# Optimization experiments

Hardware: AMD Instinct MI355X
Metric: run time of the kernel (lower is better)

Reference implementation:

```python
import jax, jax.numpy as jnp
import numpy as np

# CTBG circuit dims: units=[512,512,512], action_sz=6
UNIT1, UNIT2, UNIT3, ACTION = 512, 512, 512, 6
D_GPE_IN = UNIT1 * 3          # 1536  (striatum D1/D2/D3 blocks)
D_GPE_OUT = UNIT2 * 3         # 1536
D_GPI_IN = (UNIT1 + UNIT2) * 3  # 3072 (striatum + GPe/STN blocks)
D_GPI_OUT = UNIT2 * 3         # 1536
B = 16384


def setup_inputs() -> dict:
    key = jax.random.key(0)
    ks = jax.random.split(key, 12)
    x = jax.random.normal(ks[0], (B, D_GPE_IN), jnp.float32)
    # per-unit diagonal connectivity masks (unit_diags): [units, input_dim]
    gpe_mask = jax.random.bernoulli(ks[1], 0.5, (D_GPE_OUT, D_GPE_IN)).astype(jnp.float32)
    gpi_mask = jax.random.bernoulli(ks[2], 0.5, (D_GPI_OUT, D_GPI_IN)).astype(jnp.float32)
    # non-negative weights, uniform [0, 0.01) as in the TF initializer
    gpe_w = jax.random.uniform(ks[3], (D_GPE_IN, D_GPE_OUT), jnp.float32, 0.0, 0.01)
    gpe_b = jnp.zeros((D_GPE_OUT,), jnp.float32)
    gpi_w = jax.random.uniform(ks[4], (D_GPI_IN, D_GPI_OUT), jnp.float32, 0.0, 0.01)
    gpi_b = jnp.zeros((D_GPI_OUT,), jnp.float32)
    # Motor_cortex dense stack
    w1 = jax.random.normal(ks[5], (D_GPI_OUT, UNIT3), jnp.float32) / np.sqrt(D_GPI_OUT)
    b1 = jnp.zeros((UNIT3,), jnp.float32)
    w2 = jax.random.normal(ks[6], (UNIT3, UNIT3), jnp.float32) / np.sqrt(UNIT3)
    b2 = jnp.zeros((UNIT3,), jnp.float32)
    w3 = jax.random.normal(ks[7], (UNIT3, ACTION), jnp.float32) / np.sqrt(UNIT3)
    b3 = jnp.zeros((ACTION,), jnp.float32)
    return {"x": x, "gpe_mask": gpe_mask, "gpe_w": gpe_w, "gpe_b": gpe_b,
            "gpi_mask": gpi_mask, "gpi_w": gpi_w, "gpi_b": gpi_b,
            "w1": w1, "b1": b1, "w2": w2, "b2": b2, "w3": w3, "b3": b3}


def _masked_layer(x, mask, w, b):
    # TF original: p = transpose(matmul(diag(mask_u), x^T)) -> [B,U,I];
    #              f = diag_part(matmul(p, w)) + b
    # algebraically: f[b,u] = sum_i mask[u,i] * x[b,i] * w[i,u] + b[u]
    # which is a plain matmul against the element-wise masked weight.
    return x @ (w * mask.T) + b


def reference(x, gpe_mask, gpe_w, gpe_b, gpi_mask, gpi_w, gpi_b,
              w1, b1, w2, b2, w3, b3):
    gpe_out = _masked_layer(x, gpe_mask, gpe_w, gpe_b)          # [B, 1536]
    gpi_in = jnp.concatenate([x, gpe_out], axis=-1)              # [B, 3072]
    gpi_out = _masked_layer(gpi_in, gpi_mask, gpi_w, gpi_b)      # [B, 1536]
    h = jax.nn.relu(gpi_out @ w1 + b1)
    h = jax.nn.relu(h @ w2 + b2)
    return jax.nn.relu(h @ w3 + b3)                              # [B, 6]
```

## Files before the change

kernel.cpp:

```cpp
#include <hip/hip_runtime.h>
#include <stdint.h>


typedef __attribute__((ext_vector_type(8))) short short8;
typedef __attribute__((ext_vector_type(4))) float floatx4;

typedef const __attribute__((address_space(1))) void* gas1_cvp;
typedef __attribute__((address_space(3))) void* gas3_vp;

__device__ __forceinline__ void load_lds16(const void* g, void* s) {
    __builtin_amdgcn_global_load_lds((gas1_cvp)g, (gas3_vp)s, 16, 0, 0);
}

__device__ __forceinline__ unsigned short f2bf(float f) {
    unsigned int u = __float_as_uint(f);
    u = u + 0x7fffu + ((u >> 16) & 1u);
    return (unsigned short)(u >> 16);
}
__device__ __forceinline__ float bf2f(unsigned short h) {
    return __uint_as_float(((unsigned int)h) << 16);
}

__global__ void convert_x_kernel(const float* __restrict__ x,
                                 unsigned short* __restrict__ xb) {
    int idx = blockIdx.x * blockDim.x + threadIdx.x;
    int e = idx * 4;
    float4 v = *(const float4*)(x + e);
    ushort4 o;
    o.x = f2bf(v.x); o.y = f2bf(v.y); o.z = f2bf(v.z); o.w = f2bf(v.w);
    *(ushort4*)(xb + e) = o;
}

__device__ __forceinline__ void dev_prep_t(
        float (*tile)[65],
        const float* __restrict__ w, const float* __restrict__ mask,
        unsigned short* __restrict__ out,
        int ldw, int ldm, int ldo, int bx, int by) {
    int n0 = bx * 64;
    int k0 = by * 64;
    int t = threadIdx.x;
    int c4 = (t & 15) * 4;
    int r  = t >> 4;

    #pragma unroll
    for (int p = 0; p < 4; ++p) {
        int kk = r + p * 16;
        float4 v = *(const float4*)(w + (size_t)(k0 + kk) * ldw + n0 + c4);
        tile[c4 + 0][kk] = v.x;
        tile[c4 + 1][kk] = v.y;
        tile[c4 + 2][kk] = v.z;
        tile[c4 + 3][kk] = v.w;
    }
    __syncthreads();
    #pragma unroll
    for (int p = 0; p < 4; ++p) {
        int nn = r + p * 16;
        float mx = 1.f, my = 1.f, mz = 1.f, mw = 1.f;
        if (mask) {
            float4 m = *(const float4*)(mask + (size_t)(n0 + nn) * ldm + k0 + c4);
            mx = m.x; my = m.y; mz = m.z; mw = m.w;
        }
        ushort4 o;
        o.x = f2bf(tile[nn][c4 + 0] * mx);
        o.y = f2bf(tile[nn][c4 + 1] * my);
        o.z = f2bf(tile[nn][c4 + 2] * mz);
        o.w = f2bf(tile[nn][c4 + 3] * mw);
        *(ushort4*)(out + (size_t)(n0 + nn) * ldo + k0 + c4) = o;
    }
}

__device__ __forceinline__ void dev_prep_nt(
        float (*tile)[65],
        const float* __restrict__ w, const float* __restrict__ mask,
        unsigned short* __restrict__ out,
        int ldw, int ldm, int ldo, int bx, int by) {
    int j0 = bx * 64;
    int i0 = by * 64;
    int t = threadIdx.x;
    int c4 = (t & 15) * 4;
    int r  = t >> 4;

    #pragma unroll
    for (int p = 0; p < 4; ++p) {
        int jj = r + p * 16;
        float4 m = *(const float4*)(mask + (size_t)(j0 + jj) * ldm + i0 + c4);
        tile[c4 + 0][jj] = m.x;
        tile[c4 + 1][jj] = m.y;
        tile[c4 + 2][jj] = m.z;
        tile[c4 + 3][jj] = m.w;
    }
    __syncthreads();
    #pragma unroll
    for (int p = 0; p < 4; ++p) {
        int ii = r + p * 16;
        float4 v = *(const float4*)(w + (size_t)(i0 + ii) * ldw + j0 + c4);
        ushort4 o;
        o.x = f2bf(v.x * tile[ii][c4 + 0]);
        o.y = f2bf(v.y * tile[ii][c4 + 1]);
        o.z = f2bf(v.z * tile[ii][c4 + 2]);
        o.w = f2bf(v.w * tile[ii][c4 + 3]);
        *(ushort4*)(out + (size_t)(i0 + ii) * ldo + j0 + c4) = o;
    }
}

__global__ __launch_bounds__(256) void prep_all_kernel(
        const float* __restrict__ gpe_w, const float* __restrict__ gpe_mask,
        const float* __restrict__ gpi_w, const float* __restrict__ gpi_mask,
        const float* __restrict__ w1, const float* __restrict__ w2,
        unsigned short* __restrict__ wi_topnt, unsigned short* __restrict__ wi_bot,
        unsigned short* __restrict__ we_nt, unsigned short* __restrict__ w1t,
        unsigned short* __restrict__ w2t) {
    __shared__ float tile[64][65];
    int b = blockIdx.x;
    if (b < 576) {
        dev_prep_nt(tile, gpi_w, gpi_mask, wi_topnt, 1536, 3072, 1536,
                    b % 24, b / 24);
    } else if (b < 1152) {
        int lb = b - 576;
        dev_prep_t(tile, gpi_w + (size_t)1536 * 1536, gpi_mask + 1536, wi_bot,
                   1536, 3072, 1536, lb % 24, lb / 24);
    } else if (b < 1728) {
        int lb = b - 1152;
        dev_prep_nt(tile, gpe_w, gpe_mask, we_nt, 1536, 1536, 1536,
                    lb % 24, lb / 24);
    } else if (b < 1920) {
        int lb = b - 1728;
        dev_prep_t(tile, w1, nullptr, w1t, 512, 0, 1536, lb % 8, lb / 8);
    } else {
        int lb = b - 1920;
        dev_prep_t(tile, w2, nullptr, w2t, 512, 0, 512, lb % 8, lb / 8);
    }
}

__global__ void bvec_kernel(const float* __restrict__ avec,
                            const float* __restrict__ base,
                            const unsigned short* __restrict__ wbt,
                            float* __restrict__ outv, int K, int ld) {
    int u = blockIdx.x * 4 + (threadIdx.x >> 6);
    int lane = threadIdx.x & 63;
    const unsigned short* rowp = wbt + (size_t)u * ld;
    float s = 0.f;
    for (int j = lane; j < K; j += 64) s += avec[j] * bf2f(rowp[j]);
    #pragma unroll
    for (int off = 32; off; off >>= 1) s += __shfl_down(s, off, 64);
    if (lane == 0) outv[u] = base[u] + s;
}

template <int BMODE>
__global__ __launch_bounds__(256) void gemm64_kernel(
        const unsigned short* __restrict__ A,
        const unsigned short* __restrict__ Bt,
        const float* __restrict__ bias,
        const unsigned short* __restrict__ Add,
        unsigned short* __restrict__ C,
        int K, int lda, int ldc) {
    __shared__ unsigned short As[64 * 32];
    __shared__ unsigned short Bs[64 * 32];

    const int m0 = blockIdx.y * 64;
    const int n0 = blockIdx.x * 64;
    const int t    = threadIdx.x;
    const int lane = t & 63;
    const int w    = t >> 6;
    const int wm   = w >> 1;
    const int wn   = w & 1;
    const int lm   = lane & 15;
    const int lq   = lane >> 4;

    const int srow = lane >> 2;
    const int scol = (lane & 3) * 8;
    const unsigned short* ag = A  + (size_t)(m0 + w * 16 + srow) * lda + scol;
    const unsigned short* bg = Bt + (size_t)(n0 + w * 16 + srow) * K + scol;
    unsigned short* sA = As + w * 512;
    unsigned short* sB = Bs + w * 512;

    const unsigned short* arp[2];
    const unsigned short* brp[2];
    #pragma unroll
    for (int i = 0; i < 2; ++i) {
        arp[i] = As + (wm * 32 + i * 16 + lm) * 32 + lq * 8;
        brp[i] = Bs + (wn * 32 + i * 16 + lm) * 32 + lq * 8;
    }

    floatx4 acc[2][2] = {};

    for (int k0 = 0; k0 < K; k0 += 32) {
        __syncthreads();
        load_lds16(ag + k0, sA);
        load_lds16(bg + k0, sB);
        __syncthreads();

        short8 af[2], bf8[2];
        #pragma unroll
        for (int i = 0; i < 2; ++i) {
            af[i]  = *(const short8*)arp[i];
            bf8[i] = *(const short8*)brp[i];
        }
        #pragma unroll
        for (int mi = 0; mi < 2; ++mi)
            #pragma unroll
            for (int ni = 0; ni < 2; ++ni)
                acc[mi][ni] = __builtin_amdgcn_mfma_f32_16x16x32_bf16(
                    af[mi], bf8[ni], acc[mi][ni], 0, 0, 0);
    }

    float bv[2] = {0.f, 0.f};
    if (BMODE == 0) {
        #pragma unroll
        for (int ni = 0; ni < 2; ++ni) bv[ni] = bias[n0 + wn * 32 + ni * 16 + lm];
    }

    #pragma unroll
    for (int mi = 0; mi < 2; ++mi) {
        int rbase = m0 + wm * 32 + mi * 16 + lq * 4;
        #pragma unroll
        for (int ni = 0; ni < 2; ++ni) {
            int cc = n0 + wn * 32 + ni * 16 + lm;
            #pragma unroll
            for (int r = 0; r < 4; ++r) {
                float v = acc[mi][ni][r];
                if (BMODE == 1) v += bf2f(Add[(size_t)(rbase + r) * ldc + cc]);
                if (BMODE == 0) v += bv[ni];
                C[(size_t)(rbase + r) * ldc + cc] = f2bf(v);
            }
        }
    }
}

template <bool RELU>
__global__ __launch_bounds__(256) void gemm_bt_kernel(
        const unsigned short* __restrict__ A,
        const unsigned short* __restrict__ Bt,
        const float* __restrict__ bias,
        unsigned short* __restrict__ C,
        int K, int lda, int ldc) {
    __shared__ unsigned short As[128 * 32];
    __shared__ unsigned short Bs[128 * 32];

    const int m0 = blockIdx.y * 128;
    const int n0 = blockIdx.x * 128;
    const int t    = threadIdx.x;
    const int lane = t & 63;
    const int w    = t >> 6;
    const int wm   = w >> 1;
    const int wn   = w & 1;
    const int lm   = lane & 15;
    const int lq   = lane >> 4;

    const int srow = lane >> 2;
    const int scol = (lane & 3) * 8;
    const unsigned short* ag0 = A  + (size_t)(m0 + w * 16 + srow) * lda + scol;
    const unsigned short* ag1 = A  + (size_t)(m0 + (4 + w) * 16 + srow) * lda + scol;
    const unsigned short* bg0 = Bt + (size_t)(n0 + w * 16 + srow) * K + scol;
    const unsigned short* bg1 = Bt + (size_t)(n0 + (4 + w) * 16 + srow) * K + scol;
    unsigned short* sA0 = As + w * 512;
    unsigned short* sA1 = As + (4 + w) * 512;
    unsigned short* sB0 = Bs + w * 512;
    unsigned short* sB1 = Bs + (4 + w) * 512;

    const unsigned short* arp[4];
    const unsigned short* brp[4];
    #pragma unroll
    for (int i = 0; i < 4; ++i) {
        arp[i] = As + (wm * 64 + i * 16 + lm) * 32 + lq * 8;
        brp[i] = Bs + (wn * 64 + i * 16 + lm) * 32 + lq * 8;
    }

    floatx4 acc[4][4] = {};

    for (int k0 = 0; k0 < K; k0 += 32) {
        __syncthreads();
        load_lds16(ag0 + k0, sA0);
        load_lds16(ag1 + k0, sA1);
        load_lds16(bg0 + k0, sB0);
        load_lds16(bg1 + k0, sB1);
        __syncthreads();

        short8 af[4], bf8[4];
        #pragma unroll
        for (int i = 0; i < 4; ++i) {
            af[i]  = *(const short8*)arp[i];
            bf8[i] = *(const short8*)brp[i];
        }
        #pragma unroll
        for (int mi = 0; mi < 4; ++mi)
            #pragma unroll
            for (int ni = 0; ni < 4; ++ni)
                acc[mi][ni] = __builtin_amdgcn_mfma_f32_16x16x32_bf16(
                    af[mi], bf8[ni], acc[mi][ni], 0, 0, 0);
    }

    float bv[4];
    #pragma unroll
    for (int ni = 0; ni < 4; ++ni) bv[ni] = bias[n0 + wn * 64 + ni * 16 + lm];

    #pragma unroll
    for (int mi = 0; mi < 4; ++mi) {
        int rbase = m0 + wm * 64 + mi * 16 + lq * 4;
        #pragma unroll
        for (int ni = 0; ni < 4; ++ni) {
            int cc = n0 + wn * 64 + ni * 16 + lm;
            #pragma unroll
            for (int r = 0; r < 4; ++r) {
                float v = acc[mi][ni][r] + bv[ni];
                if (RELU) v = fmaxf(v, 0.f);
                C[(size_t)(rbase + r) * ldc + cc] = f2bf(v);
            }
        }
    }
}

__global__ void head_kernel(const unsigned short* __restrict__ h,
                            const float* __restrict__ w3,
                            const float* __restrict__ b3,
                            float* __restrict__ out) {
    int row = blockIdx.x * 4 + (threadIdx.x >> 6);
    int lane = threadIdx.x & 63;
    const unsigned short* hp = h + (size_t)row * 512 + lane * 8;
    ushort4 ha = *(const ushort4*)(hp);
    ushort4 hb = *(const ushort4*)(hp + 4);
    float hv[8] = {bf2f(ha.x), bf2f(ha.y), bf2f(ha.z), bf2f(ha.w),
                   bf2f(hb.x), bf2f(hb.y), bf2f(hb.z), bf2f(hb.w)};
    const float* wp = w3 + lane * 48;
    float s[6] = {0.f, 0.f, 0.f, 0.f, 0.f, 0.f};
    #pragma unroll
    for (int j = 0; j < 8; ++j)
        #pragma unroll
        for (int a = 0; a < 6; ++a)
            s[a] += hv[j] * wp[j * 6 + a];
    #pragma unroll
    for (int a = 0; a < 6; ++a)
        #pragma unroll
        for (int off = 32; off; off >>= 1)
            s[a] += __shfl_down(s[a], off, 64);
    if (lane == 0) {
        #pragma unroll
        for (int a = 0; a < 6; ++a)
            out[(size_t)row * 6 + a] = fmaxf(s[a] + b3[a], 0.f);
    }
}

extern "C" void kernel_launch(void* const* d_in, const int* in_sizes, int n_in,
                              void* d_out, int out_size, void* d_ws, size_t ws_size,
                              hipStream_t stream) {
    const float* x        = (const float*)d_in[0];
    const float* gpe_mask = (const float*)d_in[1];
    const float* gpe_w    = (const float*)d_in[2];
    const float* gpe_b    = (const float*)d_in[3];
    const float* gpi_mask = (const float*)d_in[4];
    const float* gpi_w    = (const float*)d_in[5];
    const float* gpi_b    = (const float*)d_in[6];
    const float* w1       = (const float*)d_in[7];
    const float* b1       = (const float*)d_in[8];
    const float* w2       = (const float*)d_in[9];
    const float* b2       = (const float*)d_in[10];
    const float* w3       = (const float*)d_in[11];
    const float* b3       = (const float*)d_in[12];
    float* out = (float*)d_out;

    char* ws = (char*)d_ws;
    unsigned short* xb        = (unsigned short*)(ws);
    unsigned short* h1        = (unsigned short*)(ws + 50331648);
    unsigned short* h2        = (unsigned short*)(ws + 67108864);
    unsigned short* wi_topnt  = (unsigned short*)(ws + 83886080);
    unsigned short* wi_bot    = (unsigned short*)(ws + 88604672);
    unsigned short* we_nt     = (unsigned short*)(ws + 93323264);
    unsigned short* wc_nt     = (unsigned short*)(ws + 98041856);
    unsigned short* w1t       = (unsigned short*)(ws + 102760448);
    unsigned short* w2t       = (unsigned short*)(ws + 104333312);
    unsigned short* w1ct      = (unsigned short*)(ws + 104857600);
    float*          bc        = (float*)(ws + 106430464);
    float*          b1c       = (float*)(ws + 106436608);

    convert_x_kernel<<<dim3(16384 * 1536 / 4 / 256), dim3(256), 0, stream>>>(x, xb);
    prep_all_kernel<<<dim3(1984), dim3(256), 0, stream>>>(
        gpe_w, gpe_mask, gpi_w, gpi_mask, w1, w2,
        wi_topnt, wi_bot, we_nt, w1t, w2t);

    bvec_kernel<<<dim3(384), dim3(256), 0, stream>>>(gpe_b, gpi_b, wi_bot, bc, 1536, 1536);
    bvec_kernel<<<dim3(128), dim3(256), 0, stream>>>(bc, b1, w1t, b1c, 1536, 1536);

    gemm64_kernel<1><<<dim3(24, 24), dim3(256), 0, stream>>>(
        we_nt, wi_bot, nullptr, wi_topnt, wc_nt, 1536, 1536, 1536);
    gemm64_kernel<2><<<dim3(24, 8), dim3(256), 0, stream>>>(
        w1t, wc_nt, nullptr, nullptr, w1ct, 1536, 1536, 1536);

    gemm_bt_kernel<true><<<dim3(4, 128), dim3(256), 0, stream>>>(
        xb, w1ct, b1c, h1, 1536, 1536, 512);
    gemm_bt_kernel<true><<<dim3(4, 128), dim3(256), 0, stream>>>(
        h1, w2t, b2, h2, 512, 512, 512);
    head_kernel<<<dim3(16384 / 4), dim3(256), 0, stream>>>(h2, w3, b3, out);
}
```

Measured before the change: 352.7 us.

## Fuse x fp32-to-bf16 conversion into first GEMM and merge small launches

Removes the separate pass that converts x to bf16. The first big GEMM now loads fp32 x directly, converts it in registers and writes it to LDS, which avoids writing and rereading a 50MB bf16 copy. The two bias-vector kernels are merged into the weight-combination GEMM launches as extra blocks, cutting the launch count. The trade-off is that the A loads become synchronous register loads rather than async LDS loads, and the main GEMM now reads twice as many bytes for A, each tile being reread by the 4 N-blocks.

```diff
diff --git a/kernel.cpp b/kernel.cpp
--- a/kernel.cpp
+++ b/kernel.cpp
@@ -20,15 +20,13 @@
 __device__ __forceinline__ float bf2f(unsigned short h) {
     return __uint_as_float(((unsigned int)h) << 16);
 }
-
-__global__ void convert_x_kernel(const float* __restrict__ x,
-                                 unsigned short* __restrict__ xb) {
-    int idx = blockIdx.x * blockDim.x + threadIdx.x;
-    int e = idx * 4;
-    float4 v = *(const float4*)(x + e);
-    ushort4 o;
-    o.x = f2bf(v.x); o.y = f2bf(v.y); o.z = f2bf(v.z); o.w = f2bf(v.w);
-    *(ushort4*)(xb + e) = o;
+__device__ __forceinline__ short8 cvt8(float4 a, float4 b) {
+    short8 r;
+    r[0] = (short)f2bf(a.x); r[1] = (short)f2bf(a.y);
+    r[2] = (short)f2bf(a.z); r[3] = (short)f2bf(a.w);
+    r[4] = (short)f2bf(b.x); r[5] = (short)f2bf(b.y);
+    r[6] = (short)f2bf(b.z); r[7] = (short)f2bf(b.w);
+    return r;
 }
 
 __device__ __forceinline__ void dev_prep_t(
@@ -132,11 +130,11 @@
     }
 }
 
-__global__ void bvec_kernel(const float* __restrict__ avec,
-                            const float* __restrict__ base,
-                            const unsigned short* __restrict__ wbt,
-                            float* __restrict__ outv, int K, int ld) {
-    int u = blockIdx.x * 4 + (threadIdx.x >> 6);
+__device__ __forceinline__ void dev_bvec(
+        const float* __restrict__ avec, const float* __restrict__ base,
+        const unsigned short* __restrict__ wbt, float* __restrict__ outv,
+        int K, int ld, int blk) {
+    int u = blk * 4 + (threadIdx.x >> 6);
     int lane = threadIdx.x & 63;
     const unsigned short* rowp = wbt + (size_t)u * ld;
     float s = 0.f;
@@ -147,18 +145,15 @@
 }
 
 template <int BMODE>
-__global__ __launch_bounds__(256) void gemm64_kernel(
+__device__ __forceinline__ void dev_gemm64(
+        unsigned short* As, unsigned short* Bs,
         const unsigned short* __restrict__ A,
         const unsigned short* __restrict__ Bt,
-        const float* __restrict__ bias,
         const unsigned short* __restrict__ Add,
         unsigned short* __restrict__ C,
-        int K, int lda, int ldc) {
-    __shared__ unsigned short As[64 * 32];
-    __shared__ unsigned short Bs[64 * 32];
-
-    const int m0 = blockIdx.y * 64;
-    const int n0 = blockIdx.x * 64;
+        int K, int lda, int ldc, int bx, int by) {
+    const int m0 = by * 64;
+    const int n0 = bx * 64;
     const int t    = threadIdx.x;
     const int lane = t & 63;
     const int w    = t >> 6;
@@ -204,12 +199,6 @@
                     af[mi], bf8[ni], acc[mi][ni], 0, 0, 0);
     }
 
-    float bv[2] = {0.f, 0.f};
-    if (BMODE == 0) {
-        #pragma unroll
-        for (int ni = 0; ni < 2; ++ni) bv[ni] = bias[n0 + wn * 32 + ni * 16 + lm];
-    }
-
     #pragma unroll
     for (int mi = 0; mi < 2; ++mi) {
         int rbase = m0 + wm * 32 + mi * 16 + lq * 4;
@@ -220,14 +209,132 @@
             for (int r = 0; r < 4; ++r) {
                 float v = acc[mi][ni][r];
                 if (BMODE == 1) v += bf2f(Add[(size_t)(rbase + r) * ldc + cc]);
-                if (BMODE == 0) v += bv[ni];
                 C[(size_t)(rbase + r) * ldc + cc] = f2bf(v);
             }
         }
     }
 }
 
-template <bool RELU>
+__global__ __launch_bounds__(256) void combo1_kernel(
+        const unsigned short* __restrict__ we_nt,
+        const unsigned short* __restrict__ wi_bot,
+        const unsigned short* __restrict__ wi_topnt,
+        unsigned short* __restrict__ wc_nt,
+        const float* __restrict__ gpe_b, const float* __restrict__ gpi_b,
+        float* __restrict__ bc) {
+    __shared__ unsigned short As[64 * 32];
+    __shared__ unsigned short Bs[64 * 32];
+    int b = blockIdx.x;
+    if (b < 576) {
+        dev_gemm64<1>(As, Bs, we_nt, wi_bot, wi_topnt, wc_nt,
+                      1536, 1536, 1536, b % 24, b / 24);
+    } else {
+        dev_bvec(gpe_b, gpi_b, wi_bot, bc, 1536, 1536, b - 576);
+    }
+}
+
+__global__ __launch_bounds__(256) void combo2_kernel(
+        const unsigned short* __restrict__ w1t,
+        const unsigned short* __restrict__ wc_nt,
+        unsigned short* __restrict__ w1ct,
+        const float* __restrict__ bc, const float* __restrict__ b1,
+        float* __restrict__ b1c) {
+    __shared__ unsigned short As[64 * 32];
+    __shared__ unsigned short Bs[64 * 32];
+    int b = blockIdx.x;
+    if (b < 192) {
+        dev_gemm64<2>(As, Bs, w1t, wc_nt, nullptr, w1ct,
+                      1536, 1536, 1536, b % 24, b / 24);
+    } else {
+        dev_bvec(bc, b1, w1t, b1c, 1536, 1536, b - 192);
+    }
+}
+
+__global__ __launch_bounds__(256) void gemm_a32_kernel(
+        const float* __restrict__ A,
+        const unsigned short* __restrict__ Bt,
+        const float* __restrict__ bias,
+        unsigned short* __restrict__ C,
+        int K, int lda, int ldc) {
+    __shared__ unsigned short As[128 * 32];
+    __shared__ unsigned short Bs[128 * 32];
+
+    const int m0 = blockIdx.y * 128;
+    const int n0 = blockIdx.x * 128;
+    const int t    = threadIdx.x;
+    const int lane = t & 63;
+    const int w    = t >> 6;
+    const int wm   = w >> 1;
+    const int wn   = w & 1;
+    const int lm   = lane & 15;
+    const int lq   = lane >> 4;
+
+    const int srow = lane >> 2;
+    const int scol = (lane & 3) * 8;
+    const float* axg0 = A + (size_t)(m0 + w * 16 + srow) * lda + scol;
+    const float* axg1 = A + (size_t)(m0 + (4 + w) * 16 + srow) * lda + scol;
+    const unsigned short* bg0 = Bt + (size_t)(n0 + w * 16 + srow) * K + scol;
+    const unsigned short* bg1 = Bt + (size_t)(n0 + (4 + w) * 16 + srow) * K + scol;
+    unsigned short* sA0w = As + (w * 16 + srow) * 32 + scol;
+    unsigned short* sA1w = As + ((4 + w) * 16 + srow) * 32 + scol;
+    unsigned short* sB0 = Bs + w * 512;
+    unsigned short* sB1 = Bs + (4 + w) * 512;
+
+    const unsigned short* arp[4];
+    const unsigned short* brp[4];
+    #pragma unroll
+    for (int i = 0; i < 4; ++i) {
+        arp[i] = As + (wm * 64 + i * 16 + lm) * 32 + lq * 8;
+        brp[i] = Bs + (wn * 64 + i * 16 + lm) * 32 + lq * 8;
+    }
+
+    floatx4 acc[4][4] = {};
+
+    for (int k0 = 0; k0 < K; k0 += 32) {
+        float4 a00 = *(const float4*)(axg0 + k0);
+        float4 a01 = *(const float4*)(axg0 + k0 + 4);
+        float4 a10 = *(const float4*)(axg1 + k0);
+        float4 a11 = *(const float4*)(axg1 + k0 + 4);
+        __syncthreads();
+        load_lds16(bg0 + k0, sB0);
+        load_lds16(bg1 + k0, sB1);
+        *(short8*)sA0w = cvt8(a00, a01);
+        *(short8*)sA1w = cvt8(a10, a11);
+        __syncthreads();
+
+        short8 af[4], bf8[4];
+        #pragma unroll
+        for (int i = 0; i < 4; ++i) {
+            af[i]  = *(const short8*)arp[i];
+            bf8[i] = *(const short8*)brp[i];
+        }
+        #pragma unroll
+        for (int mi = 0; mi < 4; ++mi)
+            #pragma unroll
+            for (int ni = 0; ni < 4; ++ni)
+                acc[mi][ni] = __builtin_amdgcn_mfma_f32_16x16x32_bf16(
+                    af[mi], bf8[ni], acc[mi][ni], 0, 0, 0);
+    }
+
+    float bv[4];
+    #pragma unroll
+    for (int ni = 0; ni < 4; ++ni) bv[ni] = bias[n0 + wn * 64 + ni * 16 + lm];
+
+    #pragma unroll
+    for (int mi = 0; mi < 4; ++mi) {
+        int rbase = m0 + wm * 64 + mi * 16 + lq * 4;
+        #pragma unroll
+        for (int ni = 0; ni < 4; ++ni) {
+            int cc = n0 + wn * 64 + ni * 16 + lm;
+            #pragma unroll
+            for (int r = 0; r < 4; ++r) {
+                float v = fmaxf(acc[mi][ni][r] + bv[ni], 0.f);
+                C[(size_t)(rbase + r) * ldc + cc] = f2bf(v);
+            }
+        }
+    }
+}
+
 __global__ __launch_bounds__(256) void gemm_bt_kernel(
         const unsigned short* __restrict__ A,
         const unsigned short* __restrict__ Bt,
@@ -302,8 +409,7 @@
             int cc = n0 + wn * 64 + ni * 16 + lm;
             #pragma unroll
             for (int r = 0; r < 4; ++r) {
-                float v = acc[mi][ni][r] + bv[ni];
-                if (RELU) v = fmaxf(v, 0.f);
+                float v = fmaxf(acc[mi][ni][r] + bv[ni], 0.f);
                 C[(size_t)(rbase + r) * ldc + cc] = f2bf(v);
             }
         }
@@ -359,35 +465,31 @@
     float* out = (float*)d_out;
 
     char* ws = (char*)d_ws;
-    unsigned short* xb        = (unsigned short*)(ws);
-    unsigned short* h1        = (unsigned short*)(ws + 50331648);
-    unsigned short* h2        = (unsigned short*)(ws + 67108864);
-    unsigned short* wi_topnt  = (unsigned short*)(ws + 83886080);
-    unsigned short* wi_bot    = (unsigned short*)(ws + 88604672);
-    unsigned short* we_nt     = (unsigned short*)(ws + 93323264);
-    unsigned short* wc_nt     = (unsigned short*)(ws + 98041856);
-    unsigned short* w1t       = (unsigned short*)(ws + 102760448);
-    unsigned short* w2t       = (unsigned short*)(ws + 104333312);
-    unsigned short* w1ct      = (unsigned short*)(ws + 104857600);
-    float*          bc        = (float*)(ws + 106430464);
-    float*          b1c       = (float*)(ws + 106436608);
-
-    convert_x_kernel<<<dim3(16384 * 1536 / 4 / 256), dim3(256), 0, stream>>>(x, xb);
+    unsigned short* h1        = (unsigned short*)(ws);
+    unsigned short* h2        = (unsigned short*)(ws + 16777216);
+    unsigned short* wi_topnt  = (unsigned short*)(ws + 33554432);
+    unsigned short* wi_bot    = (unsigned short*)(ws + 38273024);
+    unsigned short* we_nt     = (unsigned short*)(ws + 42991616);
+    unsigned short* wc_nt     = (unsigned short*)(ws + 47710208);
+    unsigned short* w1t       = (unsigned short*)(ws + 52428800);
+    unsigned short* w2t       = (unsigned short*)(ws + 54001664);
+    unsigned short* w1ct      = (unsigned short*)(ws + 54525952);
+    float*          bc        = (float*)(ws + 56098816);
+    float*          b1c       = (float*)(ws + 56104960);
+
     prep_all_kernel<<<dim3(1984), dim3(256), 0, stream>>>(
         gpe_w, gpe_mask, gpi_w, gpi_mask, w1, w2,
         wi_topnt, wi_bot, we_nt, w1t, w2t);
 
-    bvec_kernel<<<dim3(384), dim3(256), 0, stream>>>(gpe_b, gpi_b, wi_bot, bc, 1536, 1536);
-    bvec_kernel<<<dim3(128), dim3(256), 0, stream>>>(bc, b1, w1t, b1c, 1536, 1536);
-
-    gemm64_kernel<1><<<dim3(24, 24), dim3(256), 0, stream>>>(
-        we_nt, wi_bot, nullptr, wi_topnt, wc_nt, 1536, 1536, 1536);
-    gemm64_kernel<2><<<dim3(24, 8), dim3(256), 0, stream>>>(
-        w1t, wc_nt, nullptr, nullptr, w1ct, 1536, 1536, 1536);
-
-    gemm_bt_kernel<true><<<dim3(4, 128), dim3(256), 0, stream>>>(
-        xb, w1ct, b1c, h1, 1536, 1536, 512);
-    gemm_bt_kernel<true><<<dim3(4, 128), dim3(256), 0, stream>>>(
+    combo1_kernel<<<dim3(960), dim3(256), 0, stream>>>(
+        we_nt, wi_bot, wi_topnt, wc_nt, gpe_b, gpi_b, bc);
+
+    combo2_kernel<<<dim3(320), dim3(256), 0, stream>>>(
+        w1t, wc_nt, w1ct, bc, b1, b1c);
+
+    gemm_a32_kernel<<<dim3(4, 128), dim3(256), 0, stream>>>(
+        x, w1ct, b1c, h1, 1536, 1536, 512);
+    gemm_bt_kernel<<<dim3(4, 128), dim3(256), 0, stream>>>(
         h1, w2t, b2, h2, 512, 512, 512);
     head_kernel<<<dim3(16384 / 4), dim3(256), 0, stream>>>(h2, w3, b3, out);
 }
```

After: 334.4 us. -5.2%, faster.
